# Optimization experiments

Measured on AMD Instinct MI355X. Metric: run time of the kernel, lower is better.

Reference implementation:

```python
import jax, jax.numpy as jnp
import numpy as np

IN_CH, OUT_CH = 32, 32
MODES1, MODES2 = 16, 16
B, L, H, W = 8, 16, 64, 33


def setup_inputs() -> dict:
    key = jax.random.key(0)
    k = jax.random.split(key, 6)
    scale = 1.0 / (IN_CH * OUT_CH)
    wshape = (IN_CH, OUT_CH, MODES1, MODES2)
    return {
        "x_re": jax.random.normal(k[0], (B, L, IN_CH, H, W), dtype=jnp.float32),
        "x_im": jax.random.normal(k[1], (B, L, IN_CH, H, W), dtype=jnp.float32),
        "w1_re": scale * jax.random.normal(k[2], wshape, dtype=jnp.float32),
        "w1_im": scale * jax.random.normal(k[3], wshape, dtype=jnp.float32),
        "w2_re": scale * jax.random.normal(k[4], wshape, dtype=jnp.float32),
        "w2_im": scale * jax.random.normal(k[5], wshape, dtype=jnp.float32),
    }


def _mul2d(x, w):
    # x: [B, L, C_in, m1, m2] complex; w: [C_in, C_out, m1, m2] complex
    return jnp.einsum("blcij,coij->bloij", x, w)


def reference(x_re, x_im, w1_re, w1_im, w2_re, w2_im):
    x = jax.lax.complex(x_re, x_im)          # [B, L, C, H, W] complex64
    w1 = jax.lax.complex(w1_re, w1_im)       # [C_in, C_out, m1, m2]
    w2 = jax.lax.complex(w2_re, w2_im)
    Bx, Lx, Cx, Hx, Wx = x.shape
    m1 = min(Hx, MODES1)
    m2 = min(Wx, MODES2)

    out = jnp.zeros((Bx, Lx, OUT_CH, Hx, Wx), dtype=x.dtype)
    # low positive frequencies (top-left corner)
    out = out.at[:, :, :, :m1, :m2].set(
        _mul2d(x[:, :, :, :m1, :m2], w1[:, :, :m1, :m2]))
    # low negative frequencies along H (bottom-left corner)
    if Hx > 1 and (Hx > MODES1 or Wx > MODES2):
        out = out.at[:, :, :, -m1:, :m2].set(
            _mul2d(x[:, :, :, -m1:, :m2], w2[:, :, :m1, :m2]))
    # return complex result as trailing real/imag dim (float32)
    return jnp.stack([out.real, out.imag], axis=-1)
```

## Files before the change

kernel.cpp:

```cpp
#include <hip/hip_runtime.h>

#define HW 2112L
typedef float f32x4 __attribute__((ext_vector_type(4)));
typedef short s16x8 __attribute__((ext_vector_type(8)));

#define WT_PLANE 1048576L
#define OFF_WHR 0L
#define OFF_WLR (WT_PLANE)
#define OFF_WHI (2*WT_PLANE)
#define OFF_WLI (3*WT_PLANE)

__device__ __forceinline__ ushort f2bf(float f) {
    unsigned u = __float_as_uint(f);
    u += 0x7FFF + ((u >> 16) & 1);
    return (ushort)(u >> 16);
}
__device__ __forceinline__ void split_bf(float v, ushort& hi, ushort& lo) {
    hi = f2bf(v);
    float hf = __uint_as_float(((unsigned)hi) << 16);
    lo = f2bf(v - hf);
}

__global__ __launch_bounds__(256) void w_prep(
    const float* __restrict__ w1_re, const float* __restrict__ w1_im,
    const float* __restrict__ w2_re, const float* __restrict__ w2_im,
    char* __restrict__ ws)
{
    const int tid = threadIdx.x, bid = blockIdx.x;
    const int r = bid >> 5, i = (bid >> 1) & 15, nt = bid & 1;
    const float* wre = r ? w2_re : w1_re;
    const float* wim = r ? w2_im : w1_im;
    const int col = tid >> 4, j = tid & 15, o = nt * 16 + col;
    const int modeLin = (r * 16 + i) * 16 + j;
    s16x8* phr = (s16x8*)(ws + OFF_WHR);
    s16x8* plr = (s16x8*)(ws + OFF_WLR);
    s16x8* phi = (s16x8*)(ws + OFF_WHI);
    s16x8* pli = (s16x8*)(ws + OFF_WLI);
    #pragma unroll
    for (int kg = 0; kg < 4; ++kg) {
        s16x8 hr, lr, hi2, li2;
        #pragma unroll
        for (int e = 0; e < 8; ++e) {
            int c = kg * 8 + e;
            long src = ((long)(c * 32 + o) * 16 + i) * 16 + j;
            ushort a, b;
            split_bf(wre[src], a, b); hr[e] = (short)a; lr[e] = (short)b;
            split_bf(wim[src], a, b); hi2[e] = (short)a; li2[e] = (short)b;
        }
        long off = (long)(modeLin * 2 + nt) * 64 + kg * 16 + col;
        phr[off] = hr; plr[off] = lr; phi[off] = hi2; pli[off] = li2;
    }
}

__global__ __launch_bounds__(256, 6) void k2_compute(
    const float* __restrict__ x_re, const float* __restrict__ x_im,
    float* __restrict__ out, const char* __restrict__ ws)
{
    const int tid = threadIdx.x, bid = blockIdx.x;

    __shared__ __align__(16) ushort xfr[16][4][32];
    __shared__ __align__(16) ushort xfi[16][4][32];
    __shared__ __align__(16) float2 stg[128][17];

    if (bid >= 1024) {
        const int fid = bid - 1024;
        int gtid = fid * 256 + tid, n = 256 * 256;
        float4* out4 = (float4*)out;
        const float4 z = make_float4(0.f, 0.f, 0.f, 0.f);
        for (int idx = gtid; idx < 4096 * 528; idx += n) {
            int plane = idx / 528;
            int k = idx - plane * 528;
            out4[(long)plane * 1056 + 264 + k] = z;
        }
        return;
    }

    const int r = bid >> 9, i = (bid >> 5) & 15, bt = bid & 31;
    const int h = r ? 48 + i : i;
    const int bl0 = bt * 4;
    const int modeBase = (r * 16 + i) * 16;

    #pragma unroll
    for (int p = 0; p < 2; ++p) {
        int idx = p * 256 + tid;
        int j4 = idx & 3, row = idx >> 2;
        int c = row >> 2, bl = row & 3;
        long base = ((long)((bl0 + bl) * 32 + c)) * HW + h * 33 + j4 * 4;
        float re0 = x_re[base + 0], re1 = x_re[base + 1], re2 = x_re[base + 2], re3 = x_re[base + 3];
        float im0 = x_im[base + 0], im1 = x_im[base + 1], im2 = x_im[base + 2], im3 = x_im[base + 3];
        xfr[j4 * 4 + 0][bl][c] = f2bf(re0); xfi[j4 * 4 + 0][bl][c] = f2bf(im0);
        xfr[j4 * 4 + 1][bl][c] = f2bf(re1); xfi[j4 * 4 + 1][bl][c] = f2bf(im1);
        xfr[j4 * 4 + 2][bl][c] = f2bf(re2); xfi[j4 * 4 + 2][bl][c] = f2bf(im2);
        xfr[j4 * 4 + 3][bl][c] = f2bf(re3); xfi[j4 * 4 + 3][bl][c] = f2bf(im3);
    }
    __syncthreads();

    const int wave = tid >> 6, lane = tid & 63;
    const int m = lane & 3, ks = lane >> 4, colo = lane & 15;

    const s16x8* Bwhr = (const s16x8*)(ws + OFF_WHR);
    const s16x8* Bwlr = (const s16x8*)(ws + OFF_WLR);
    const s16x8* Bwhi = (const s16x8*)(ws + OFF_WHI);
    const s16x8* Bwli = (const s16x8*)(ws + OFF_WLI);

    #pragma unroll
    for (int jj = 0; jj < 4; ++jj) {
        const int j = wave * 4 + jj;
        const int modeLin = modeBase + j;

        s16x8 Ahr = *(const s16x8*)&xfr[j][m][ks * 8];
        s16x8 Ahi = *(const s16x8*)&xfi[j][m][ks * 8];

        #pragma unroll
        for (int nt = 0; nt < 2; ++nt) {
            long boff = (long)(modeLin * 2 + nt) * 64 + lane;
            s16x8 Bhr = Bwhr[boff], Blr = Bwlr[boff];
            s16x8 Bhi = Bwhi[boff], Bli = Bwli[boff];

            f32x4 accP = (f32x4)0.0f, accN = (f32x4)0.0f, accI = (f32x4)0.0f;
            accP = __builtin_amdgcn_mfma_f32_16x16x32_bf16(Ahr, Bhr, accP, 0, 0, 0);
            accP = __builtin_amdgcn_mfma_f32_16x16x32_bf16(Ahr, Blr, accP, 0, 0, 0);
            accN = __builtin_amdgcn_mfma_f32_16x16x32_bf16(Ahi, Bhi, accN, 0, 0, 0);
            accN = __builtin_amdgcn_mfma_f32_16x16x32_bf16(Ahi, Bli, accN, 0, 0, 0);
            accI = __builtin_amdgcn_mfma_f32_16x16x32_bf16(Ahr, Bhi, accI, 0, 0, 0);
            accI = __builtin_amdgcn_mfma_f32_16x16x32_bf16(Ahr, Bli, accI, 0, 0, 0);
            accI = __builtin_amdgcn_mfma_f32_16x16x32_bf16(Ahi, Bhr, accI, 0, 0, 0);
            accI = __builtin_amdgcn_mfma_f32_16x16x32_bf16(Ahi, Blr, accI, 0, 0, 0);

            if (ks == 0) {
                #pragma unroll
                for (int q = 0; q < 4; ++q)
                    stg[q * 32 + nt * 16 + colo][j] =
                        make_float2(accP[q] - accN[q], accI[q]);
            }
        }
    }
    __syncthreads();

    float2* out2 = (float2*)out;
    #pragma unroll 2
    for (int t = 0; t < 17; ++t) {
        int idx = t * 256 + tid;
        if (idx < 128 * 33) {
            int row = idx / 33;
            int k = idx - row * 33;
            float2 v = (k < 16) ? stg[row][k] : make_float2(0.f, 0.f);
            long dst = ((long)(bl0 * 32 + row) * 64 + h) * 33 + k;
            out2[dst] = v;
        }
    }
}

extern "C" void kernel_launch(void* const* d_in, const int* in_sizes, int n_in,
                              void* d_out, int out_size, void* d_ws, size_t ws_size,
                              hipStream_t stream) {
    const float* x_re  = (const float*)d_in[0];
    const float* x_im  = (const float*)d_in[1];
    const float* w1_re = (const float*)d_in[2];
    const float* w1_im = (const float*)d_in[3];
    const float* w2_re = (const float*)d_in[4];
    const float* w2_im = (const float*)d_in[5];
    float* out = (float*)d_out;
    char* ws = (char*)d_ws;

    w_prep<<<dim3(64), dim3(256), 0, stream>>>(w1_re, w1_im, w2_re, w2_im, ws);
    k2_compute<<<dim3(1280), dim3(256), 0, stream>>>(x_re, x_im, out, ws);
}
```

Baseline: 34.94 us.

## Split zero-fill into own kernel, prefetch weights, widen weight prep grid

Moves the middle-region zero fill out of the compute kernel into a separate fill_mid launch. The compute kernel now issues its first weight loads before the x staging and prefetches the next mode's weights while the MFMAs of the current mode run, so global-load latency can overlap. It also reorders blocks so the 64 blocks that share a mode row run next to each other, and doubles the w_prep grid by splitting the K groups. The cost is an extra kernel launch, higher register pressure from the prefetch buffers (the occupancy hint drops from 6 to 4), and the fill no longer overlapping the compute in a single launch.

```diff
diff --git a/kernel.cpp b/kernel.cpp
--- a/kernel.cpp
+++ b/kernel.cpp
@@ -27,7 +27,7 @@
     char* __restrict__ ws)
 {
     const int tid = threadIdx.x, bid = blockIdx.x;
-    const int r = bid >> 5, i = (bid >> 1) & 15, nt = bid & 1;
+    const int r = bid >> 6, i = (bid >> 2) & 15, nt = (bid >> 1) & 1, kh = bid & 1;
     const float* wre = r ? w2_re : w1_re;
     const float* wim = r ? w2_im : w1_im;
     const int col = tid >> 4, j = tid & 15, o = nt * 16 + col;
@@ -37,7 +37,8 @@
     s16x8* phi = (s16x8*)(ws + OFF_WHI);
     s16x8* pli = (s16x8*)(ws + OFF_WLI);
     #pragma unroll
-    for (int kg = 0; kg < 4; ++kg) {
+    for (int kk = 0; kk < 2; ++kk) {
+        const int kg = kh * 2 + kk;
         s16x8 hr, lr, hi2, li2;
         #pragma unroll
         for (int e = 0; e < 8; ++e) {
@@ -52,33 +53,48 @@
     }
 }
 
-__global__ __launch_bounds__(256, 6) void k2_compute(
+__global__ __launch_bounds__(256) void fill_mid(float* __restrict__ out) {
+    int gtid = blockIdx.x * 256 + threadIdx.x, n = 1024 * 256;
+    float4* out4 = (float4*)out;
+    const float4 z = make_float4(0.f, 0.f, 0.f, 0.f);
+    for (int idx = gtid; idx < 4096 * 528; idx += n) {
+        int plane = idx / 528;
+        int k = idx - plane * 528;
+        out4[(long)plane * 1056 + 264 + k] = z;
+    }
+}
+
+__global__ __launch_bounds__(256, 4) void k3_compute(
     const float* __restrict__ x_re, const float* __restrict__ x_im,
     float* __restrict__ out, const char* __restrict__ ws)
 {
     const int tid = threadIdx.x, bid = blockIdx.x;
+    const int g = bid & 63, i = bid >> 6;
+    const int r = g >> 5, bt = g & 31;
+    const int h = r ? 48 + i : i;
+    const int bl0 = bt * 4;
+    const int modeBase = (r * 16 + i) * 16;
 
     __shared__ __align__(16) ushort xfr[16][4][32];
     __shared__ __align__(16) ushort xfi[16][4][32];
     __shared__ __align__(16) float2 stg[128][17];
 
-    if (bid >= 1024) {
-        const int fid = bid - 1024;
-        int gtid = fid * 256 + tid, n = 256 * 256;
-        float4* out4 = (float4*)out;
-        const float4 z = make_float4(0.f, 0.f, 0.f, 0.f);
-        for (int idx = gtid; idx < 4096 * 528; idx += n) {
-            int plane = idx / 528;
-            int k = idx - plane * 528;
-            out4[(long)plane * 1056 + 264 + k] = z;
-        }
-        return;
+    const int wave = tid >> 6, lane = tid & 63;
+    const int m = lane & 3, ks = lane >> 4, colo = lane & 15;
+
+    const s16x8* Bwhr = (const s16x8*)(ws + OFF_WHR);
+    const s16x8* Bwlr = (const s16x8*)(ws + OFF_WLR);
+    const s16x8* Bwhi = (const s16x8*)(ws + OFF_WHI);
+    const s16x8* Bwli = (const s16x8*)(ws + OFF_WLI);
+
+    const int j0 = wave * 4;
+    s16x8 cBhr[2], cBlr[2], cBhi[2], cBli[2];
+    {
+        long b0 = ((long)(modeBase + j0) * 2 + 0) * 64 + lane;
+        long b1 = ((long)(modeBase + j0) * 2 + 1) * 64 + lane;
+        cBhr[0] = Bwhr[b0]; cBlr[0] = Bwlr[b0]; cBhi[0] = Bwhi[b0]; cBli[0] = Bwli[b0];
+        cBhr[1] = Bwhr[b1]; cBlr[1] = Bwlr[b1]; cBhi[1] = Bwhi[b1]; cBli[1] = Bwli[b1];
     }
-
-    const int r = bid >> 9, i = (bid >> 5) & 15, bt = bid & 31;
-    const int h = r ? 48 + i : i;
-    const int bl0 = bt * 4;
-    const int modeBase = (r * 16 + i) * 16;
 
     #pragma unroll
     for (int p = 0; p < 2; ++p) {
@@ -95,43 +111,46 @@
     }
     __syncthreads();
 
-    const int wave = tid >> 6, lane = tid & 63;
-    const int m = lane & 3, ks = lane >> 4, colo = lane & 15;
-
-    const s16x8* Bwhr = (const s16x8*)(ws + OFF_WHR);
-    const s16x8* Bwlr = (const s16x8*)(ws + OFF_WLR);
-    const s16x8* Bwhi = (const s16x8*)(ws + OFF_WHI);
-    const s16x8* Bwli = (const s16x8*)(ws + OFF_WLI);
-
     #pragma unroll
     for (int jj = 0; jj < 4; ++jj) {
-        const int j = wave * 4 + jj;
-        const int modeLin = modeBase + j;
+        const int j = j0 + jj;
+
+        s16x8 nBhr[2], nBlr[2], nBhi[2], nBli[2];
+        if (jj < 3) {
+            long b0 = ((long)(modeBase + j + 1) * 2 + 0) * 64 + lane;
+            long b1 = ((long)(modeBase + j + 1) * 2 + 1) * 64 + lane;
+            nBhr[0] = Bwhr[b0]; nBlr[0] = Bwlr[b0]; nBhi[0] = Bwhi[b0]; nBli[0] = Bwli[b0];
+            nBhr[1] = Bwhr[b1]; nBlr[1] = Bwlr[b1]; nBhi[1] = Bwhi[b1]; nBli[1] = Bwli[b1];
+        }
 
         s16x8 Ahr = *(const s16x8*)&xfr[j][m][ks * 8];
         s16x8 Ahi = *(const s16x8*)&xfi[j][m][ks * 8];
 
         #pragma unroll
         for (int nt = 0; nt < 2; ++nt) {
-            long boff = (long)(modeLin * 2 + nt) * 64 + lane;
-            s16x8 Bhr = Bwhr[boff], Blr = Bwlr[boff];
-            s16x8 Bhi = Bwhi[boff], Bli = Bwli[boff];
-
             f32x4 accP = (f32x4)0.0f, accN = (f32x4)0.0f, accI = (f32x4)0.0f;
-            accP = __builtin_amdgcn_mfma_f32_16x16x32_bf16(Ahr, Bhr, accP, 0, 0, 0);
-            accP = __builtin_amdgcn_mfma_f32_16x16x32_bf16(Ahr, Blr, accP, 0, 0, 0);
-            accN = __builtin_amdgcn_mfma_f32_16x16x32_bf16(Ahi, Bhi, accN, 0, 0, 0);
-            accN = __builtin_amdgcn_mfma_f32_16x16x32_bf16(Ahi, Bli, accN, 0, 0, 0);
-            accI = __builtin_amdgcn_mfma_f32_16x16x32_bf16(Ahr, Bhi, accI, 0, 0, 0);
-            accI = __builtin_amdgcn_mfma_f32_16x16x32_bf16(Ahr, Bli, accI, 0, 0, 0);
-            accI = __builtin_amdgcn_mfma_f32_16x16x32_bf16(Ahi, Bhr, accI, 0, 0, 0);
-            accI = __builtin_amdgcn_mfma_f32_16x16x32_bf16(Ahi, Blr, accI, 0, 0, 0);
+            accP = __builtin_amdgcn_mfma_f32_16x16x32_bf16(Ahr, cBhr[nt], accP, 0, 0, 0);
+            accP = __builtin_amdgcn_mfma_f32_16x16x32_bf16(Ahr, cBlr[nt], accP, 0, 0, 0);
+            accN = __builtin_amdgcn_mfma_f32_16x16x32_bf16(Ahi, cBhi[nt], accN, 0, 0, 0);
+            accN = __builtin_amdgcn_mfma_f32_16x16x32_bf16(Ahi, cBli[nt], accN, 0, 0, 0);
+            accI = __builtin_amdgcn_mfma_f32_16x16x32_bf16(Ahr, cBhi[nt], accI, 0, 0, 0);
+            accI = __builtin_amdgcn_mfma_f32_16x16x32_bf16(Ahr, cBli[nt], accI, 0, 0, 0);
+            accI = __builtin_amdgcn_mfma_f32_16x16x32_bf16(Ahi, cBhr[nt], accI, 0, 0, 0);
+            accI = __builtin_amdgcn_mfma_f32_16x16x32_bf16(Ahi, cBlr[nt], accI, 0, 0, 0);
 
             if (ks == 0) {
                 #pragma unroll
                 for (int q = 0; q < 4; ++q)
                     stg[q * 32 + nt * 16 + colo][j] =
                         make_float2(accP[q] - accN[q], accI[q]);
+            }
+        }
+
+        if (jj < 3) {
+            #pragma unroll
+            for (int nt = 0; nt < 2; ++nt) {
+                cBhr[nt] = nBhr[nt]; cBlr[nt] = nBlr[nt];
+                cBhi[nt] = nBhi[nt]; cBli[nt] = nBli[nt];
             }
         }
     }
@@ -163,6 +182,7 @@
     float* out = (float*)d_out;
     char* ws = (char*)d_ws;
 
-    w_prep<<<dim3(64), dim3(256), 0, stream>>>(w1_re, w1_im, w2_re, w2_im, ws);
-    k2_compute<<<dim3(1280), dim3(256), 0, stream>>>(x_re, x_im, out, ws);
+    w_prep<<<dim3(128), dim3(256), 0, stream>>>(w1_re, w1_im, w2_re, w2_im, ws);
+    fill_mid<<<dim3(1024), dim3(256), 0, stream>>>(out);
+    k3_compute<<<dim3(1024), dim3(256), 0, stream>>>(x_re, x_im, out, ws);
 }
```

Measured after the change: 36.49 us. 1.04x slower.

## Restructure spectral kernel per (bl, corner, out-half) with register-prefetched weights

Applied to the files above, without the earlier changes.

Moves the bf16 hi/lo split from the weights to the activations, so weights are stored only as bf16 hi parts. The main kernel is reorganised so each block owns one batch-time slice, one frequency corner and one half of the output channels. It loops over 16 mode rows in chunks of four, prefetching the next row's weights into registers and overlapping each chunk's output stores with the next chunk's loads. Zero-fill of the non-mode region is folded into the same blocks instead of separate filler blocks. This cuts the grid to 512 larger blocks at occupancy hint 2. The trade-off is lower parallelism and higher register pressure, and each x row is now read by two blocks, one per output half.

```diff
diff --git a/kernel.cpp b/kernel.cpp
--- a/kernel.cpp
+++ b/kernel.cpp
@@ -1,24 +1,14 @@
 #include <hip/hip_runtime.h>
 
-#define HW 2112L
 typedef float f32x4 __attribute__((ext_vector_type(4)));
 typedef short s16x8 __attribute__((ext_vector_type(8)));
 
-#define WT_PLANE 1048576L
-#define OFF_WHR 0L
-#define OFF_WLR (WT_PLANE)
-#define OFF_WHI (2*WT_PLANE)
-#define OFF_WLI (3*WT_PLANE)
+#define MFMA(a, b, c) __builtin_amdgcn_mfma_f32_16x16x32_bf16(a, b, c, 0, 0, 0)
 
 __device__ __forceinline__ ushort f2bf(float f) {
     unsigned u = __float_as_uint(f);
     u += 0x7FFF + ((u >> 16) & 1);
     return (ushort)(u >> 16);
-}
-__device__ __forceinline__ void split_bf(float v, ushort& hi, ushort& lo) {
-    hi = f2bf(v);
-    float hf = __uint_as_float(((unsigned)hi) << 16);
-    lo = f2bf(v - hf);
 }
 
 __global__ __launch_bounds__(256) void w_prep(
@@ -32,121 +22,147 @@
     const float* wim = r ? w2_im : w1_im;
     const int col = tid >> 4, j = tid & 15, o = nt * 16 + col;
     const int modeLin = (r * 16 + i) * 16 + j;
-    s16x8* phr = (s16x8*)(ws + OFF_WHR);
-    s16x8* plr = (s16x8*)(ws + OFF_WLR);
-    s16x8* phi = (s16x8*)(ws + OFF_WHI);
-    s16x8* pli = (s16x8*)(ws + OFF_WLI);
+    s16x8* pb = (s16x8*)ws;
     #pragma unroll
     for (int kg = 0; kg < 4; ++kg) {
-        s16x8 hr, lr, hi2, li2;
+        s16x8 hr, hi2;
         #pragma unroll
         for (int e = 0; e < 8; ++e) {
             int c = kg * 8 + e;
             long src = ((long)(c * 32 + o) * 16 + i) * 16 + j;
-            ushort a, b;
-            split_bf(wre[src], a, b); hr[e] = (short)a; lr[e] = (short)b;
-            split_bf(wim[src], a, b); hi2[e] = (short)a; li2[e] = (short)b;
+            hr[e]  = (short)f2bf(wre[src]);
+            hi2[e] = (short)f2bf(wim[src]);
         }
-        long off = (long)(modeLin * 2 + nt) * 64 + kg * 16 + col;
-        phr[off] = hr; plr[off] = lr; phi[off] = hi2; pli[off] = li2;
+        long base = (long)(modeLin * 2 + nt) * 128;
+        pb[base + kg * 16 + col]      = hr;
+        pb[base + 64 + kg * 16 + col] = hi2;
     }
 }
 
-__global__ __launch_bounds__(256, 6) void k2_compute(
+__global__ __launch_bounds__(256, 2) void k_main(
     const float* __restrict__ x_re, const float* __restrict__ x_im,
     float* __restrict__ out, const char* __restrict__ ws)
 {
     const int tid = threadIdx.x, bid = blockIdx.x;
+    const int bl = bid & 127;
+    const int rn = bid >> 7;
+    const int r = rn & 1, nt = rn >> 1;
+    const int hbase = r ? 48 : 0;
+    const int obase = nt * 16;
+    const int modeBase0 = r * 256;
 
-    __shared__ __align__(16) ushort xfr[16][4][32];
-    __shared__ __align__(16) ushort xfi[16][4][32];
-    __shared__ __align__(16) float2 stg[128][17];
+    __shared__ ushort Afr[8192];
+    __shared__ float2 stg[2112];
 
-    if (bid >= 1024) {
-        const int fid = bid - 1024;
-        int gtid = fid * 256 + tid, n = 256 * 256;
-        float4* out4 = (float4*)out;
-        const float4 z = make_float4(0.f, 0.f, 0.f, 0.f);
-        for (int idx = gtid; idx < 4096 * 528; idx += n) {
-            int plane = idx / 528;
-            int k = idx - plane * 528;
-            out4[(long)plane * 1056 + 264 + k] = z;
-        }
-        return;
+    const int lane = tid & 63, wave = tid >> 6;
+    const int ks = lane >> 4, colo = lane & 15;
+    const s16x8* BW = (const s16x8*)ws;
+
+    s16x8 cB[8], nB[8];
+    #pragma unroll
+    for (int jj = 0; jj < 4; ++jj) {
+        long mb = (long)((modeBase0 + wave * 4 + jj) * 2 + nt) * 128;
+        cB[jj * 2 + 0] = BW[mb + lane];
+        cB[jj * 2 + 1] = BW[mb + 64 + lane];
     }
 
-    const int r = bid >> 9, i = (bid >> 5) & 15, bt = bid & 31;
-    const int h = r ? 48 + i : i;
-    const int bl0 = bt * 4;
-    const int modeBase = (r * 16 + i) * 16;
-
-    #pragma unroll
-    for (int p = 0; p < 2; ++p) {
-        int idx = p * 256 + tid;
-        int j4 = idx & 3, row = idx >> 2;
-        int c = row >> 2, bl = row & 3;
-        long base = ((long)((bl0 + bl) * 32 + c)) * HW + h * 33 + j4 * 4;
-        float re0 = x_re[base + 0], re1 = x_re[base + 1], re2 = x_re[base + 2], re3 = x_re[base + 3];
-        float im0 = x_im[base + 0], im1 = x_im[base + 1], im2 = x_im[base + 2], im3 = x_im[base + 3];
-        xfr[j4 * 4 + 0][bl][c] = f2bf(re0); xfi[j4 * 4 + 0][bl][c] = f2bf(im0);
-        xfr[j4 * 4 + 1][bl][c] = f2bf(re1); xfi[j4 * 4 + 1][bl][c] = f2bf(im1);
-        xfr[j4 * 4 + 2][bl][c] = f2bf(re2); xfi[j4 * 4 + 2][bl][c] = f2bf(im2);
-        xfr[j4 * 4 + 3][bl][c] = f2bf(re3); xfi[j4 * 4 + 3][bl][c] = f2bf(im3);
-    }
-    __syncthreads();
-
-    const int wave = tid >> 6, lane = tid & 63;
-    const int m = lane & 3, ks = lane >> 4, colo = lane & 15;
-
-    const s16x8* Bwhr = (const s16x8*)(ws + OFF_WHR);
-    const s16x8* Bwlr = (const s16x8*)(ws + OFF_WLR);
-    const s16x8* Bwhi = (const s16x8*)(ws + OFF_WHI);
-    const s16x8* Bwli = (const s16x8*)(ws + OFF_WLI);
-
-    #pragma unroll
-    for (int jj = 0; jj < 4; ++jj) {
-        const int j = wave * 4 + jj;
-        const int modeLin = modeBase + j;
-
-        s16x8 Ahr = *(const s16x8*)&xfr[j][m][ks * 8];
-        s16x8 Ahi = *(const s16x8*)&xfi[j][m][ks * 8];
+    for (int ch = 0; ch < 4; ++ch) {
+        #pragma unroll
+        for (int pass = 0; pass < 2; ++pass) {
+            int u = pass * 256 + tid;
+            int j4 = u & 3, hl = (u >> 2) & 3, c = u >> 4;
+            long sb = ((long)(bl * 32 + c) * 64 + hbase + ch * 4 + hl) * 33 + j4 * 4;
+            int la = (hl * 16 + j4 * 4) * 128 + c;
+            #pragma unroll
+            for (int q = 0; q < 4; ++q) {
+                float re = x_re[sb + q], im = x_im[sb + q];
+                ushort hr = f2bf(re);
+                ushort lr = f2bf(re - __uint_as_float((unsigned)hr << 16));
+                ushort hi = f2bf(im);
+                ushort li = f2bf(im - __uint_as_float((unsigned)hi << 16));
+                int a = la + q * 128;
+                Afr[a] = hr; Afr[a + 32] = lr; Afr[a + 64] = hi; Afr[a + 96] = li;
+            }
+        }
+        if (ch > 0) {
+            #pragma unroll 1
+            for (int t = 0; t < 9; ++t) {
+                int idx = t * 256 + tid;
+                if (idx < 2112) {
+                    int o = idx / 132;
+                    int rem = idx - o * 132;
+                    int hl = rem / 33, w = rem - hl * 33;
+                    float2 v = (w < 16) ? stg[(hl * 16 + o) * 33 + w] : make_float2(0.f, 0.f);
+                    long dst = ((long)(bl * 32 + obase + o) * 64 + hbase + (ch - 1) * 4 + hl) * 33 + w;
+                    ((float2*)out)[dst] = v;
+                }
+            }
+        }
+        __syncthreads();
 
         #pragma unroll
-        for (int nt = 0; nt < 2; ++nt) {
-            long boff = (long)(modeLin * 2 + nt) * 64 + lane;
-            s16x8 Bhr = Bwhr[boff], Blr = Bwlr[boff];
-            s16x8 Bhi = Bwhi[boff], Bli = Bwli[boff];
-
-            f32x4 accP = (f32x4)0.0f, accN = (f32x4)0.0f, accI = (f32x4)0.0f;
-            accP = __builtin_amdgcn_mfma_f32_16x16x32_bf16(Ahr, Bhr, accP, 0, 0, 0);
-            accP = __builtin_amdgcn_mfma_f32_16x16x32_bf16(Ahr, Blr, accP, 0, 0, 0);
-            accN = __builtin_amdgcn_mfma_f32_16x16x32_bf16(Ahi, Bhi, accN, 0, 0, 0);
-            accN = __builtin_amdgcn_mfma_f32_16x16x32_bf16(Ahi, Bli, accN, 0, 0, 0);
-            accI = __builtin_amdgcn_mfma_f32_16x16x32_bf16(Ahr, Bhi, accI, 0, 0, 0);
-            accI = __builtin_amdgcn_mfma_f32_16x16x32_bf16(Ahr, Bli, accI, 0, 0, 0);
-            accI = __builtin_amdgcn_mfma_f32_16x16x32_bf16(Ahi, Bhr, accI, 0, 0, 0);
-            accI = __builtin_amdgcn_mfma_f32_16x16x32_bf16(Ahi, Blr, accI, 0, 0, 0);
-
-            if (ks == 0) {
+        for (int hl = 0; hl < 4; ++hl) {
+            const int i = ch * 4 + hl;
+            if (i < 15) {
                 #pragma unroll
-                for (int q = 0; q < 4; ++q)
-                    stg[q * 32 + nt * 16 + colo][j] =
-                        make_float2(accP[q] - accN[q], accI[q]);
+                for (int jj = 0; jj < 4; ++jj) {
+                    long mb = (long)((modeBase0 + (i + 1) * 16 + wave * 4 + jj) * 2 + nt) * 128;
+                    nB[jj * 2 + 0] = BW[mb + lane];
+                    nB[jj * 2 + 1] = BW[mb + 64 + lane];
+                }
+            }
+            #pragma unroll
+            for (int jj = 0; jj < 4; ++jj) {
+                const int j = wave * 4 + jj;
+                const int ab = (hl * 16 + j) * 128 + ks * 8;
+                s16x8 Ahr = *(const s16x8*)&Afr[ab];
+                s16x8 Alr = *(const s16x8*)&Afr[ab + 32];
+                s16x8 Ahi = *(const s16x8*)&Afr[ab + 64];
+                s16x8 Ali = *(const s16x8*)&Afr[ab + 96];
+                f32x4 accP = (f32x4)0.0f, accN = (f32x4)0.0f, accI = (f32x4)0.0f;
+                accP = MFMA(Ahr, cB[jj * 2 + 0], accP);
+                accP = MFMA(Alr, cB[jj * 2 + 0], accP);
+                accN = MFMA(Ahi, cB[jj * 2 + 1], accN);
+                accN = MFMA(Ali, cB[jj * 2 + 1], accN);
+                accI = MFMA(Ahr, cB[jj * 2 + 1], accI);
+                accI = MFMA(Alr, cB[jj * 2 + 1], accI);
+                accI = MFMA(Ahi, cB[jj * 2 + 0], accI);
+                accI = MFMA(Ali, cB[jj * 2 + 0], accI);
+                if (lane < 16)
+                    stg[(hl * 16 + colo) * 33 + j] = make_float2(accP[0] - accN[0], accI[0]);
+            }
+            if (i < 15) {
+                #pragma unroll
+                for (int q = 0; q < 8; ++q) cB[q] = nB[q];
             }
         }
+        __syncthreads();
     }
-    __syncthreads();
 
-    float2* out2 = (float2*)out;
-    #pragma unroll 2
+    #pragma unroll 1
+    for (int t = 0; t < 9; ++t) {
+        int idx = t * 256 + tid;
+        if (idx < 2112) {
+            int o = idx / 132;
+            int rem = idx - o * 132;
+            int hl = rem / 33, w = rem - hl * 33;
+            float2 v = (w < 16) ? stg[(hl * 16 + o) * 33 + w] : make_float2(0.f, 0.f);
+            long dst = ((long)(bl * 32 + obase + o) * 64 + hbase + 12 + hl) * 33 + w;
+            ((float2*)out)[dst] = v;
+        }
+    }
+
+    const int f4off = ((r ? 32 : 16) * 33) >> 1;
+    float4* out4 = (float4*)out;
+    const float4 z = make_float4(0.f, 0.f, 0.f, 0.f);
+    #pragma unroll 1
     for (int t = 0; t < 17; ++t) {
         int idx = t * 256 + tid;
-        if (idx < 128 * 33) {
-            int row = idx / 33;
-            int k = idx - row * 33;
-            float2 v = (k < 16) ? stg[row][k] : make_float2(0.f, 0.f);
-            long dst = ((long)(bl0 * 32 + row) * 64 + h) * 33 + k;
-            out2[dst] = v;
+        if (idx < 4224) {
+            int o = idx >> 8;
+            o = idx / 264;
+            int q = idx - o * 264;
+            out4[(long)(bl * 32 + obase + o) * 1056 + f4off + q] = z;
         }
     }
 }
@@ -164,5 +180,5 @@
     char* ws = (char*)d_ws;
 
     w_prep<<<dim3(64), dim3(256), 0, stream>>>(w1_re, w1_im, w2_re, w2_im, ws);
-    k2_compute<<<dim3(1280), dim3(256), 0, stream>>>(x_re, x_im, out, ws);
+    k_main<<<dim3(512), dim3(256), 0, stream>>>(x_re, x_im, out, ws);
 }
```

New measurement: 49.19 us. +40.8%, slower.
